# Optimization experiments

Hardware: AMD Instinct MI355X
Metric: run time of the kernel (lower is better)

## Reference

```python
import jax, jax.numpy as jnp
import numpy as np

N, E, F_IN = 10000, 160000, 256
H1, C1 = 8, 128          # conv1: heads=8, out 128 per head, concat -> 1024
H2, C2 = 1, 64           # conv2: heads=1, out 64
NEG_SLOPE = 0.2


def setup_inputs() -> dict:
    key = jax.random.key(0)
    ks = jax.random.split(key, 10)
    s_in = 1.0 / np.sqrt(F_IN)
    s_h1 = 1.0 / np.sqrt(H1 * C1)
    return {
        "x": jax.random.normal(ks[0], (N, F_IN), dtype=jnp.float32),
        "edge_index": jax.random.randint(ks[1], (2, E), 0, N, dtype=jnp.int64),
        "W1": jax.random.normal(ks[2], (F_IN, H1 * C1), dtype=jnp.float32) * s_in,
        "att_src1": jax.random.normal(ks[3], (H1, C1), dtype=jnp.float32) * 0.1,
        "att_dst1": jax.random.normal(ks[4], (H1, C1), dtype=jnp.float32) * 0.1,
        "b1": jnp.zeros((H1 * C1,), dtype=jnp.float32),
        "W2": jax.random.normal(ks[5], (H1 * C1, H2 * C2), dtype=jnp.float32) * s_h1,
        "att_src2": jax.random.normal(ks[6], (H2, C2), dtype=jnp.float32) * 0.1,
        "att_dst2": jax.random.normal(ks[7], (H2, C2), dtype=jnp.float32) * 0.1,
        "b2": jnp.zeros((H2 * C2,), dtype=jnp.float32),
    }


def gat_conv(x, src, dst, W, att_src, att_dst, b, n):
    """PyG GATConv (eval mode: dropout off), concat=True, add_self_loops handled by caller."""
    H, C = att_src.shape
    h = (x @ W).reshape(n, H, C)                       # [N,H,C]
    a_s = jnp.einsum('nhc,hc->nh', h, att_src)         # [N,H]
    a_d = jnp.einsum('nhc,hc->nh', h, att_dst)         # [N,H]
    e = jax.nn.leaky_relu(a_s[src] + a_d[dst], NEG_SLOPE)  # [Etot,H]
    # softmax over edges grouped by destination node (numerically stable)
    e_max = jax.ops.segment_max(e, dst, num_segments=n)
    e = jnp.exp(e - e_max[dst])
    denom = jax.ops.segment_sum(e, dst, num_segments=n)
    alpha = e / (denom[dst] + 1e-16)                   # [Etot,H]
    msg = h[src] * alpha[:, :, None]                   # [Etot,H,C]
    out = jax.ops.segment_sum(msg, dst, num_segments=n)  # [N,H,C]
    return out.reshape(n, H * C) + b


def reference(x, edge_index, W1, att_src1, att_dst1, b1, W2, att_src2, att_dst2, b2):
    n = x.shape[0]
    loops = jnp.arange(n, dtype=edge_index.dtype)
    src = jnp.concatenate([edge_index[0], loops])
    dst = jnp.concatenate([edge_index[1], loops])
    h = jax.nn.elu(gat_conv(x, src, dst, W1, att_src1, att_dst1, b1, n))
    return gat_conv(h, src, dst, W2, att_src2, att_dst2, b2, n)
```

## Files before the change

### kernel.cpp

```cpp
#include <hip/hip_runtime.h>
#include <cmath>


typedef short bf16x8 __attribute__((ext_vector_type(8)));
typedef float f32x4 __attribute__((ext_vector_type(4)));
typedef unsigned short u16x8 __attribute__((ext_vector_type(8)));

__device__ __forceinline__ float lrelu(float x) { return x > 0.f ? x : 0.2f * x; }
__device__ __forceinline__ float b2f(unsigned short h) {
  return __uint_as_float(((unsigned)h) << 16);
}
__device__ __forceinline__ unsigned short f2bf(float f) {
  unsigned u = __float_as_uint(f);
  u += 0x7FFFu + ((u >> 16) & 1u);
  return (unsigned short)(u >> 16);
}

__device__ __forceinline__ void fma8(float* acc, uint4 v, float e) {
  acc[0] += e * __uint_as_float(v.x << 16);
  acc[1] += e * __uint_as_float(v.x & 0xffff0000u);
  acc[2] += e * __uint_as_float(v.y << 16);
  acc[3] += e * __uint_as_float(v.y & 0xffff0000u);
  acc[4] += e * __uint_as_float(v.z << 16);
  acc[5] += e * __uint_as_float(v.z & 0xffff0000u);
  acc[6] += e * __uint_as_float(v.w << 16);
  acc[7] += e * __uint_as_float(v.w & 0xffff0000u);
}

#define GLOAD_LDS16(gsrc, ldst)                                              \
  __builtin_amdgcn_global_load_lds(                                          \
      (const __attribute__((address_space(1))) unsigned int*)(gsrc),         \
      (__attribute__((address_space(3))) unsigned int*)(ldst), 16, 0, 0)


__global__ __launch_bounds__(256) void prep_fused(
    const int* __restrict__ ei, int* __restrict__ counts, int E,
    const float* __restrict__ x, unsigned short* __restrict__ xpk, int N, int MB1,
    const float* __restrict__ W1, unsigned short* __restrict__ w1pk,
    const float* __restrict__ W2, unsigned short* __restrict__ w2pk) {
  const int countB = (E + 255) / 256;
  const int pxB = MB1 * 8;
  int bid = blockIdx.x;
  int t = threadIdx.x;

  if (bid < countB) {
    int e = bid * 256 + t;
    if (e < E) atomicAdd(&counts[ei[E + e]], 1);
    return;
  }
  bid -= countB;
  if (bid < pxB) {
    int mb = bid >> 3, ks = bid & 7;
    int l = t & 63, f = t >> 6;
    int row = mb * 64 + f * 16 + (l & 15);
    int kc = ks * 32 + (l >> 4) * 8;
    float v[8];
#pragma unroll
    for (int j = 0; j < 8; ++j) v[j] = 0.f;
    if (row < N) {
      const float* xr = x + (size_t)row * 256 + kc;
#pragma unroll
      for (int j = 0; j < 8; ++j) v[j] = xr[j];
    }
    u16x8 hi;
#pragma unroll
    for (int j = 0; j < 8; ++j) hi[j] = f2bf(v[j]);
    size_t base = (size_t)(mb * 8 + ks) * 4 * 512;
    *(u16x8*)(xpk + base + (size_t)f * 512 + l * 8) = hi;
    return;
  }
  bid -= pxB;
  if (bid < 64) {
    int hb = bid >> 3, ks = bid & 7;
    int l = t & 63, gq = t >> 6;
    for (int g = gq; g < 8; g += 4) {
      int n = hb * 128 + g * 16 + (l & 15);
      int k0 = ks * 32 + (l >> 4) * 8;
      u16x8 hi, lo;
#pragma unroll
      for (int j = 0; j < 8; ++j) {
        float v = W1[(size_t)(k0 + j) * 1024 + n];
        unsigned short h = f2bf(v);
        hi[j] = h; lo[j] = f2bf(v - b2f(h));
      }
      size_t base = (size_t)(hb * 8 + ks) * 16 * 512;
      *(u16x8*)(w1pk + base + (size_t)g * 512 + l * 8) = hi;
      *(u16x8*)(w1pk + base + (size_t)(8 + g) * 512 + l * 8) = lo;
    }
    return;
  }
  bid -= 64;
  {
    int ks = bid;
    int l = t & 63, g = t >> 6;
    int n = g * 16 + (l & 15);
    int k0 = ks * 32 + (l >> 4) * 8;
    u16x8 hi, lo;
#pragma unroll
    for (int j = 0; j < 8; ++j) {
      float v = W2[(size_t)(k0 + j) * 64 + n];
      unsigned short h = f2bf(v);
      hi[j] = h; lo[j] = f2bf(v - b2f(h));
    }
    size_t base = (size_t)ks * 8 * 512;
    *(u16x8*)(w2pk + base + (size_t)g * 512 + l * 8) = hi;
    *(u16x8*)(w2pk + base + (size_t)(4 + g) * 512 + l * 8) = lo;
  }
}


__global__ __launch_bounds__(256) void scan_blk(const int* __restrict__ counts,
                                                int* __restrict__ offsets,
                                                int* __restrict__ bsum, int n) {
  __shared__ int lds[256];
  int b = blockIdx.x, t = threadIdx.x, i = b * 256 + t;
  int v = (i < n) ? counts[i] + 1 : 0;
  lds[t] = v;
  __syncthreads();
  for (int off = 1; off < 256; off <<= 1) {
    int tv = (t >= off) ? lds[t - off] : 0;
    __syncthreads();
    lds[t] += tv;
    __syncthreads();
  }
  if (i < n) offsets[i] = lds[t] - v;
  if (t == 255) bsum[b] = lds[255];
}

__global__ __launch_bounds__(256) void scan_apply(int* __restrict__ offsets,
                                                  int* __restrict__ cursors,
                                                  const int* __restrict__ bsum,
                                                  int nb, int n) {
  __shared__ int pre_s;
  int b = blockIdx.x, t = threadIdx.x;
  if (t == 0) {
    int s = 0;
    for (int i = 0; i < b; ++i) s += bsum[i];
    pre_s = s;
    if (b == nb - 1) {
      int tot = s;
      for (int i = b; i < nb; ++i) tot += bsum[i];
      offsets[n] = tot;
    }
  }
  __syncthreads();
  int i = b * 256 + t;
  if (i < n) {
    int o = offsets[i] + pre_s;
    offsets[i] = o;
    cursors[i] = o;
  }
}

__global__ __launch_bounds__(256) void fill_all(const int* __restrict__ ei,
                                                int* __restrict__ cursors,
                                                const int* __restrict__ offsets,
                                                int* __restrict__ list,
                                                int E, int n) {
  int tid = blockIdx.x * 256 + threadIdx.x;
  if (tid < E) {
    int d = ei[E + tid];
    int pos = atomicAdd(&cursors[d], 1);
    list[pos] = ei[tid];
  } else if (tid < E + n) {
    int i = tid - E;
    list[offsets[i + 1] - 1] = i;
  }
}


__global__ __launch_bounds__(512, 4) void gemm1_att(
    const unsigned short* __restrict__ xpk, const unsigned short* __restrict__ w1pk,
    const float* __restrict__ asrc, const float* __restrict__ adst,
    unsigned short* __restrict__ h1b, float* __restrict__ as1,
    float* __restrict__ ad1) {
  extern __shared__ char sm[];
  const int t = threadIdx.x, wid = t >> 6, lane = t & 63;
  const int wr = wid >> 2, wc = wid & 3;
  const int mb = blockIdx.x, hb = blockIdx.y;
  const int m0 = mb * 128;
  const int l15 = lane & 15, l4 = lane >> 4;

  f32x4 acc[4][2] = {};

  auto stage = [&](int buf, int ks) {
    char* base0 = sm + buf * 24576;
    for (int i = wid; i < 24; i += 8) {
      const unsigned short* src;
      int ldsoff;
      if (i < 8) {
        int r = i >> 2;
        src = xpk + (size_t)((2 * mb + r) * 8 + ks) * 2048 + (i & 3) * 512 + lane * 8;
        ldsoff = i * 1024;
      } else if (i < 16) {
        int g = i - 8;
        src = w1pk + (size_t)(hb * 8 + ks) * 8192 + g * 512 + lane * 8;
        ldsoff = 8192 + g * 1024;
      } else {
        int g = i - 16;
        src = w1pk + (size_t)(hb * 8 + ks) * 8192 + (8 + g) * 512 + lane * 8;
        ldsoff = 16384 + g * 1024;
      }
      GLOAD_LDS16(src, base0 + ldsoff);
    }
  };

  stage(0, 0);
  __syncthreads();
  int buf = 0;
  for (int step = 0; step < 8; ++step) {
    if (step < 7) stage(buf ^ 1, step + 1);
    const char* b = sm + buf * 24576;
    bf16x8 ah[4], bh[2], bl[2];
#pragma unroll
    for (int mf = 0; mf < 4; ++mf)
      ah[mf] = *(const bf16x8*)(b + (wr * 4 + mf) * 1024 + lane * 16);
#pragma unroll
    for (int nf = 0; nf < 2; ++nf) {
      bh[nf] = *(const bf16x8*)(b + 8192 + (wc * 2 + nf) * 1024 + lane * 16);
      bl[nf] = *(const bf16x8*)(b + 16384 + (wc * 2 + nf) * 1024 + lane * 16);
    }
#pragma unroll
    for (int mf = 0; mf < 4; ++mf)
#pragma unroll
      for (int nf = 0; nf < 2; ++nf) {
        acc[mf][nf] = __builtin_amdgcn_mfma_f32_16x16x32_bf16(ah[mf], bh[nf], acc[mf][nf], 0, 0, 0);
        acc[mf][nf] = __builtin_amdgcn_mfma_f32_16x16x32_bf16(ah[mf], bl[nf], acc[mf][nf], 0, 0, 0);
      }
    __syncthreads();
    buf ^= 1;
  }

  float* parts_s = (float*)sm;
  float* parts_d = (float*)(sm + 2048);
  unsigned short* ctile = (unsigned short*)(sm + 4096);
  float as_c[2], ad_c[2];
#pragma unroll
  for (int nf = 0; nf < 2; ++nf) {
    int col = hb * 128 + wc * 32 + nf * 16 + l15;
    as_c[nf] = asrc[col];
    ad_c[nf] = adst[col];
  }
#pragma unroll
  for (int mf = 0; mf < 4; ++mf) {
    float ss[4] = {0.f, 0.f, 0.f, 0.f}, dd[4] = {0.f, 0.f, 0.f, 0.f};
#pragma unroll
    for (int nf = 0; nf < 2; ++nf)
#pragma unroll
      for (int r = 0; r < 4; ++r) {
        ss[r] += acc[mf][nf][r] * as_c[nf];
        dd[r] += acc[mf][nf][r] * ad_c[nf];
      }
#pragma unroll
    for (int r = 0; r < 4; ++r)
      for (int m = 1; m < 16; m <<= 1) {
        ss[r] += __shfl_xor(ss[r], m);
        dd[r] += __shfl_xor(dd[r], m);
      }
    if (l15 == 0) {
#pragma unroll
      for (int r = 0; r < 4; ++r) {
        int row = wr * 64 + mf * 16 + l4 * 4 + r;
        parts_s[row * 4 + wc] = ss[r];
        parts_d[row * 4 + wc] = dd[r];
      }
    }
#pragma unroll
    for (int nf = 0; nf < 2; ++nf)
#pragma unroll
      for (int r = 0; r < 4; ++r) {
        int row = wr * 64 + mf * 16 + l4 * 4 + r;
        int col = wc * 32 + nf * 16 + l15;
        ctile[row * 128 + col] = f2bf(acc[mf][nf][r]);
      }
  }
  __syncthreads();
  if (t < 128) {
    float s = parts_s[t * 4] + parts_s[t * 4 + 1] + parts_s[t * 4 + 2] + parts_s[t * 4 + 3];
    float d = parts_d[t * 4] + parts_d[t * 4 + 1] + parts_d[t * 4 + 2] + parts_d[t * 4 + 3];
    as1[(size_t)(m0 + t) * 8 + hb] = s;
    ad1[(size_t)(m0 + t) * 8 + hb] = d;
  }
#pragma unroll
  for (int rep = 0; rep < 4; ++rep) {
    int e = rep * 4096 + t * 8;
    int row = e >> 7, col = e & 127;
    bf16x8 v = *(const bf16x8*)(ctile + e);
    *(bf16x8*)(h1b + (size_t)(m0 + row) * 1024 + hb * 128 + col) = v;
  }
}


__global__ __launch_bounds__(256) void agg1_gather(
    const unsigned short* __restrict__ h1b, const float* __restrict__ as1,
    const float* __restrict__ ad1, const int* __restrict__ offsets,
    const int* __restrict__ list, const float* __restrict__ b1,
    unsigned short* __restrict__ o1pk, int n, int nblk) {
  __shared__ __align__(16) unsigned short stg[8192];
  const int t = threadIdx.x, w = t >> 6, lane = t & 63;
  const int h0 = lane >> 4, h1_ = h0 + 4;

  for (int blk = blockIdx.x; blk < nblk; blk += gridDim.x) {
    const int node = blk * 4 + w;
    if (node < n) {
      const int beg = offsets[node], end = offsets[node + 1];
      const float ad0 = ad1[(size_t)node * 8 + h0];
      const float ad4 = ad1[(size_t)node * 8 + h1_];
      float acc0[8] = {}, acc1[8] = {};
      float den0 = 0.f, den4 = 0.f;

      int j = beg;
      int sA = 0, sB = 0;
      float aA0 = 0.f, aA4 = 0.f, aB0 = 0.f, aB4 = 0.f;
      uint4 vA0, vA1, vB0, vB1;
      if (j + 2 <= end) {
        sA = list[j]; sB = list[j + 1];
        aA0 = as1[(size_t)sA * 8 + h0]; aA4 = as1[(size_t)sA * 8 + h1_];
        aB0 = as1[(size_t)sB * 8 + h0]; aB4 = as1[(size_t)sB * 8 + h1_];
        vA0 = *(const uint4*)(h1b + (size_t)sA * 1024 + lane * 8);
        vA1 = *(const uint4*)(h1b + (size_t)sA * 1024 + 512 + lane * 8);
        vB0 = *(const uint4*)(h1b + (size_t)sB * 1024 + lane * 8);
        vB1 = *(const uint4*)(h1b + (size_t)sB * 1024 + 512 + lane * 8);
      }
      for (; j + 4 <= end; j += 2) {
        int sA2 = list[j + 2], sB2 = list[j + 3];
        float aA02 = as1[(size_t)sA2 * 8 + h0], aA42 = as1[(size_t)sA2 * 8 + h1_];
        float aB02 = as1[(size_t)sB2 * 8 + h0], aB42 = as1[(size_t)sB2 * 8 + h1_];
        uint4 nA0 = *(const uint4*)(h1b + (size_t)sA2 * 1024 + lane * 8);
        uint4 nA1 = *(const uint4*)(h1b + (size_t)sA2 * 1024 + 512 + lane * 8);
        uint4 nB0 = *(const uint4*)(h1b + (size_t)sB2 * 1024 + lane * 8);
        uint4 nB1 = *(const uint4*)(h1b + (size_t)sB2 * 1024 + 512 + lane * 8);
        float eA0 = __expf(lrelu(aA0 + ad0)), eA4 = __expf(lrelu(aA4 + ad4));
        float eB0 = __expf(lrelu(aB0 + ad0)), eB4 = __expf(lrelu(aB4 + ad4));
        den0 += eA0 + eB0; den4 += eA4 + eB4;
        fma8(acc0, vA0, eA0); fma8(acc1, vA1, eA4);
        fma8(acc0, vB0, eB0); fma8(acc1, vB1, eB4);
        sA = sA2; sB = sB2;
        aA0 = aA02; aA4 = aA42; aB0 = aB02; aB4 = aB42;
        vA0 = nA0; vA1 = nA1; vB0 = nB0; vB1 = nB1;
      }
      if (j + 2 <= end) {
        float eA0 = __expf(lrelu(aA0 + ad0)), eA4 = __expf(lrelu(aA4 + ad4));
        float eB0 = __expf(lrelu(aB0 + ad0)), eB4 = __expf(lrelu(aB4 + ad4));
        den0 += eA0 + eB0; den4 += eA4 + eB4;
        fma8(acc0, vA0, eA0); fma8(acc1, vA1, eA4);
        fma8(acc0, vB0, eB0); fma8(acc1, vB1, eB4);
        j += 2;
      }
      if (j < end) {
        int s = list[j];
        float a0 = as1[(size_t)s * 8 + h0], a4 = as1[(size_t)s * 8 + h1_];
        uint4 v0 = *(const uint4*)(h1b + (size_t)s * 1024 + lane * 8);
        uint4 v1 = *(const uint4*)(h1b + (size_t)s * 1024 + 512 + lane * 8);
        float e0 = __expf(lrelu(a0 + ad0)), e4 = __expf(lrelu(a4 + ad4));
        den0 += e0; den4 += e4;
        fma8(acc0, v0, e0); fma8(acc1, v1, e4);
      }

      const float inv0 = 1.f / (den0 + 1e-16f);
      const float inv4 = 1.f / (den4 + 1e-16f);
      u16x8 hiA, loA, hiB, loB;
#pragma unroll
      for (int k = 0; k < 8; ++k) {
        float vA = acc0[k] * inv0 + b1[lane * 8 + k];
        float vB = acc1[k] * inv4 + b1[512 + lane * 8 + k];
        vA = vA > 0.f ? vA : expm1f(vA);
        vB = vB > 0.f ? vB : expm1f(vB);
        unsigned short hA = f2bf(vA), hB = f2bf(vB);
        hiA[k] = hA; loA[k] = f2bf(vA - b2f(hA));
        hiB[k] = hB; loB[k] = f2bf(vB - b2f(hB));
      }
      const int q2 = lane >> 2, kc = lane & 3;
      {
        int aw = q2 * 512 + kc * 64 + w * 16;
        *(u16x8*)((char*)stg + (aw ^ ((q2 & 7) << 4))) = hiA;
        aw += 256;
        *(u16x8*)((char*)stg + (aw ^ ((q2 & 7) << 4))) = loA;
      }
      {
        int ks = 16 + q2;
        int aw = ks * 512 + kc * 64 + w * 16;
        *(u16x8*)((char*)stg + (aw ^ ((ks & 7) << 4))) = hiB;
        aw += 256;
        *(u16x8*)((char*)stg + (aw ^ ((ks & 7) << 4))) = loB;
      }
    }
    __syncthreads();
    const int mb = blk >> 4, f = (blk >> 2) & 3, l15b = (blk & 3) * 4;
#pragma unroll
    for (int it = 0; it < 4; ++it) {
      int a = it * 4096 + t * 16;
      int ks = a >> 9, half = (a >> 8) & 1, kcc = (a >> 6) & 3, ww = (a >> 4) & 3;
      u16x8 v = *(const u16x8*)((const char*)stg + (a ^ ((ks & 7) << 4)));
      size_t g = (size_t)(mb * 32 + ks) * 4096 + half * 2048 + (size_t)f * 512 +
                 (size_t)(kcc * 16 + l15b + ww) * 8;
      *(u16x8*)(o1pk + g) = v;
    }
    __syncthreads();
  }
}


__global__ __launch_bounds__(256) void gemm2_splitk(
    const unsigned short* __restrict__ o1pk, const unsigned short* __restrict__ w2pk,
    float* __restrict__ h2p, int Mpad) {
  extern __shared__ char sm[];
  const int t = threadIdx.x, wid = t >> 6, lane = t & 63;
  const int wr = wid >> 1, wc = wid & 1;
  const int mb = blockIdx.x, sk = blockIdx.y;
  const int m0 = mb * 64;
  const int l15 = lane & 15, l4 = lane >> 4;

  f32x4 acc[2][2] = {};

  auto stage = [&](int buf, int ks) {
    char* base0 = sm + buf * 16384;
    const unsigned short* ax = o1pk + (size_t)(mb * 32 + ks) * 8 * 512 + lane * 8;
    for (int i = wid; i < 8; i += 4)
      GLOAD_LDS16(ax + i * 512, base0 + i * 1024);
    const unsigned short* bw = w2pk + (size_t)ks * 8 * 512 + lane * 8;
    for (int i = wid; i < 8; i += 4)
      GLOAD_LDS16(bw + i * 512, base0 + 8192 + i * 1024);
  };

  stage(0, sk * 8);
  __syncthreads();
  int buf = 0;
  for (int step = 0; step < 8; ++step) {
    if (step < 7) stage(buf ^ 1, sk * 8 + step + 1);
    const char* b = sm + buf * 16384;
    bf16x8 ah[2], al[2], bh[2], bl[2];
#pragma unroll
    for (int mf = 0; mf < 2; ++mf) {
      int f = wr * 2 + mf;
      ah[mf] = *(const bf16x8*)(b + f * 1024 + lane * 16);
      al[mf] = *(const bf16x8*)(b + 4096 + f * 1024 + lane * 16);
    }
#pragma unroll
    for (int nf = 0; nf < 2; ++nf) {
      int g = wc * 2 + nf;
      bh[nf] = *(const bf16x8*)(b + 8192 + g * 1024 + lane * 16);
      bl[nf] = *(const bf16x8*)(b + 12288 + g * 1024 + lane * 16);
    }
#pragma unroll
    for (int mf = 0; mf < 2; ++mf)
#pragma unroll
      for (int nf = 0; nf < 2; ++nf) {
        acc[mf][nf] = __builtin_amdgcn_mfma_f32_16x16x32_bf16(ah[mf], bh[nf], acc[mf][nf], 0, 0, 0);
        acc[mf][nf] = __builtin_amdgcn_mfma_f32_16x16x32_bf16(ah[mf], bl[nf], acc[mf][nf], 0, 0, 0);
        acc[mf][nf] = __builtin_amdgcn_mfma_f32_16x16x32_bf16(al[mf], bh[nf], acc[mf][nf], 0, 0, 0);
      }
    __syncthreads();
    buf ^= 1;
  }

#pragma unroll
  for (int mf = 0; mf < 2; ++mf)
#pragma unroll
    for (int nf = 0; nf < 2; ++nf)
#pragma unroll
      for (int r = 0; r < 4; ++r) {
        int row = wr * 32 + mf * 16 + l4 * 4 + r;
        int col = wc * 32 + nf * 16 + l15;
        h2p[((size_t)sk * Mpad + m0 + row) * 64 + col] = acc[mf][nf][r];
      }
}


__global__ __launch_bounds__(256) void reduce_att2(
    const float* __restrict__ h2p, const float* __restrict__ asrc,
    const float* __restrict__ adst, float* __restrict__ h2,
    float* __restrict__ as2, float* __restrict__ ad2, int Mpad, int n) {
  int w = threadIdx.x >> 6, lane = threadIdx.x & 63;
  int row = blockIdx.x * 4 + w;
  if (row >= n) return;
  float s = 0.f;
#pragma unroll
  for (int sk = 0; sk < 4; ++sk) s += h2p[((size_t)sk * Mpad + row) * 64 + lane];
  h2[(size_t)row * 64 + lane] = s;
  float ds = s * asrc[lane], dd = s * adst[lane];
  for (int o = 32; o; o >>= 1) { ds += __shfl_xor(ds, o); dd += __shfl_xor(dd, o); }
  if (lane == 0) { as2[row] = ds; ad2[row] = dd; }
}


__global__ __launch_bounds__(256) void agg2_gather(
    const float* __restrict__ h2, const float* __restrict__ as2,
    const float* __restrict__ ad2, const int* __restrict__ offsets,
    const int* __restrict__ list, const float* __restrict__ b2,
    float* __restrict__ out, int n, int nblk) {
  const int wid = threadIdx.x >> 6, lane = threadIdx.x & 63;
  const int cb = (lane & 15) * 4;
  const int jo = lane >> 4;

  for (int blk = blockIdx.x; blk < nblk; blk += gridDim.x) {
    const int node = blk * 4 + wid;
    if (node >= n) continue;
    const int beg = offsets[node], end = offsets[node + 1];
    const float ad = ad2[node];

    float4 acc = make_float4(0.f, 0.f, 0.f, 0.f);
    float den = 0.f;
    for (int j = beg + jo; j < end; j += 4) {
      int s = list[j];
      float e = __expf(lrelu(as2[s] + ad));
      den += e;
      float4 v = *(const float4*)&h2[(size_t)s * 64 + cb];
      acc.x += e * v.x; acc.y += e * v.y; acc.z += e * v.z; acc.w += e * v.w;
    }
    acc.x += __shfl_xor(acc.x, 16); acc.y += __shfl_xor(acc.y, 16);
    acc.z += __shfl_xor(acc.z, 16); acc.w += __shfl_xor(acc.w, 16);
    den += __shfl_xor(den, 16);
    acc.x += __shfl_xor(acc.x, 32); acc.y += __shfl_xor(acc.y, 32);
    acc.z += __shfl_xor(acc.z, 32); acc.w += __shfl_xor(acc.w, 32);
    den += __shfl_xor(den, 32);
    if (jo == 0) {
      float inv = 1.f / (den + 1e-16f);
      float4 r;
      r.x = acc.x * inv + b2[cb];
      r.y = acc.y * inv + b2[cb + 1];
      r.z = acc.z * inv + b2[cb + 2];
      r.w = acc.w * inv + b2[cb + 3];
      *(float4*)&out[(size_t)node * 64 + cb] = r;
    }
  }
}


extern "C" void kernel_launch(void* const* d_in, const int* in_sizes, int n_in,
                              void* d_out, int out_size, void* d_ws, size_t ws_size,
                              hipStream_t stream) {
  const float* x     = (const float*)d_in[0];
  const int*   ei    = (const int*)d_in[1];
  const float* W1    = (const float*)d_in[2];
  const float* asrc1 = (const float*)d_in[3];
  const float* adst1 = (const float*)d_in[4];
  const float* b1    = (const float*)d_in[5];
  const float* W2    = (const float*)d_in[6];
  const float* asrc2 = (const float*)d_in[7];
  const float* adst2 = (const float*)d_in[8];
  const float* b2    = (const float*)d_in[9];
  float* out = (float*)d_out;

  const int N = in_sizes[0] / 256;
  const int E = in_sizes[1] / 2;
  const int T = E + N;
  const int MBB = (N + 127) / 128;
  const int Mpad = MBB * 128;
  const int MB1 = Mpad / 64;
  const int NB = (N + 255) / 256;
  const int NBLK4 = (N + 3) / 4;
  const int AGG_GRID = NBLK4 < 2048 ? NBLK4 : 2048;

  char* p = (char*)d_ws;
  auto bump = [&](size_t bytes) {
    char* r = p;
    p += (bytes + 255) & ~(size_t)255;
    return r;
  };
  int* counts  = (int*)bump((size_t)N * 4);
  int* offsets = (int*)bump((size_t)(N + 1) * 4);
  int* cursors = (int*)bump((size_t)N * 4);
  int* bsum    = (int*)bump((size_t)NB * 4);
  int* list    = (int*)bump((size_t)T * 4);
  unsigned short* xpk  = (unsigned short*)bump((size_t)Mpad * 256 * 2);
  unsigned short* w1pk = (unsigned short*)bump((size_t)8 * 8 * 16 * 512 * 2);
  unsigned short* h1b  = (unsigned short*)bump((size_t)Mpad * 1024 * 2);
  float* as1           = (float*)bump((size_t)Mpad * 8 * 4);
  float* ad1           = (float*)bump((size_t)Mpad * 8 * 4);
  unsigned short* o1pk = (unsigned short*)bump((size_t)Mpad * 2048 * 2);
  unsigned short* w2pk = (unsigned short*)bump((size_t)32 * 8 * 512 * 2);
  float* as2           = (float*)bump((size_t)Mpad * 4);
  float* ad2           = (float*)bump((size_t)Mpad * 4);
  float* h2p = (float*)h1b;
  float* h2  = (float*)xpk;

  hipMemsetAsync(counts, 0, (size_t)N * 4, stream);
  {
    int gridsz = (E + 255) / 256 + MB1 * 8 + 64 + 32;
    prep_fused<<<gridsz, 256, 0, stream>>>(ei, counts, E, x, xpk, N, MB1,
                                           W1, w1pk, W2, w2pk);
  }
  scan_blk<<<NB, 256, 0, stream>>>(counts, offsets, bsum, N);
  scan_apply<<<NB, 256, 0, stream>>>(offsets, cursors, bsum, NB, N);
  fill_all<<<(E + N + 255) / 256, 256, 0, stream>>>(ei, cursors, offsets, list, E, N);

  gemm1_att<<<dim3(MBB, 8), 512, 49152, stream>>>(xpk, w1pk, asrc1, adst1, h1b, as1, ad1);
  agg1_gather<<<AGG_GRID, 256, 0, stream>>>(h1b, as1, ad1, offsets, list, b1, o1pk, N, NBLK4);

  gemm2_splitk<<<dim3(Mpad / 64, 4), 256, 32768, stream>>>(o1pk, w2pk, h2p, Mpad);
  reduce_att2<<<(N + 3) / 4, 256, 0, stream>>>(h2p, asrc2, adst2, h2, as2, ad2, Mpad, N);
  agg2_gather<<<AGG_GRID, 256, 0, stream>>>(h2, as2, ad2, offsets, list, b2, out, N, NBLK4);
}
```

Before: 156.2 us.

## Replace split-bf16 compensated GEMMs with single-pass fp16 MFMA

```diff
diff --git a/kernel.cpp b/kernel.cpp
--- a/kernel.cpp
+++ b/kernel.cpp
@@ -2,29 +2,28 @@
 #include <cmath>
 
 
-typedef short bf16x8 __attribute__((ext_vector_type(8)));
+typedef _Float16 f16x8 __attribute__((ext_vector_type(8)));
 typedef float f32x4 __attribute__((ext_vector_type(4)));
 typedef unsigned short u16x8 __attribute__((ext_vector_type(8)));
 
 __device__ __forceinline__ float lrelu(float x) { return x > 0.f ? x : 0.2f * x; }
-__device__ __forceinline__ float b2f(unsigned short h) {
-  return __uint_as_float(((unsigned)h) << 16);
-}
-__device__ __forceinline__ unsigned short f2bf(float f) {
-  unsigned u = __float_as_uint(f);
-  u += 0x7FFFu + ((u >> 16) & 1u);
-  return (unsigned short)(u >> 16);
-}
-
-__device__ __forceinline__ void fma8(float* acc, uint4 v, float e) {
-  acc[0] += e * __uint_as_float(v.x << 16);
-  acc[1] += e * __uint_as_float(v.x & 0xffff0000u);
-  acc[2] += e * __uint_as_float(v.y << 16);
-  acc[3] += e * __uint_as_float(v.y & 0xffff0000u);
-  acc[4] += e * __uint_as_float(v.z << 16);
-  acc[5] += e * __uint_as_float(v.z & 0xffff0000u);
-  acc[6] += e * __uint_as_float(v.w << 16);
-  acc[7] += e * __uint_as_float(v.w & 0xffff0000u);
+__device__ __forceinline__ unsigned short f2h(float f) {
+  _Float16 h = (_Float16)f;
+  return __builtin_bit_cast(unsigned short, h);
+}
+__device__ __forceinline__ float h2f(unsigned short u) {
+  return (float)__builtin_bit_cast(_Float16, u);
+}
+
+__device__ __forceinline__ void fma8h(float* acc, uint4 v, float e) {
+  acc[0] += e * h2f((unsigned short)(v.x & 0xffffu));
+  acc[1] += e * h2f((unsigned short)(v.x >> 16));
+  acc[2] += e * h2f((unsigned short)(v.y & 0xffffu));
+  acc[3] += e * h2f((unsigned short)(v.y >> 16));
+  acc[4] += e * h2f((unsigned short)(v.z & 0xffffu));
+  acc[5] += e * h2f((unsigned short)(v.z >> 16));
+  acc[6] += e * h2f((unsigned short)(v.w & 0xffffu));
+  acc[7] += e * h2f((unsigned short)(v.w >> 16));
 }
 
 #define GLOAD_LDS16(gsrc, ldst)                                              \
@@ -62,11 +61,11 @@
 #pragma unroll
       for (int j = 0; j < 8; ++j) v[j] = xr[j];
     }
-    u16x8 hi;
-#pragma unroll
-    for (int j = 0; j < 8; ++j) hi[j] = f2bf(v[j]);
-    size_t base = (size_t)(mb * 8 + ks) * 4 * 512;
-    *(u16x8*)(xpk + base + (size_t)f * 512 + l * 8) = hi;
+    u16x8 hv;
+#pragma unroll
+    for (int j = 0; j < 8; ++j) hv[j] = f2h(v[j]);
+    size_t base = (size_t)(mb * 8 + ks) * 2048;
+    *(u16x8*)(xpk + base + (size_t)f * 512 + l * 8) = hv;
     return;
   }
   bid -= pxB;
@@ -76,16 +75,11 @@
     for (int g = gq; g < 8; g += 4) {
       int n = hb * 128 + g * 16 + (l & 15);
       int k0 = ks * 32 + (l >> 4) * 8;
-      u16x8 hi, lo;
-#pragma unroll
-      for (int j = 0; j < 8; ++j) {
-        float v = W1[(size_t)(k0 + j) * 1024 + n];
-        unsigned short h = f2bf(v);
-        hi[j] = h; lo[j] = f2bf(v - b2f(h));
-      }
-      size_t base = (size_t)(hb * 8 + ks) * 16 * 512;
-      *(u16x8*)(w1pk + base + (size_t)g * 512 + l * 8) = hi;
-      *(u16x8*)(w1pk + base + (size_t)(8 + g) * 512 + l * 8) = lo;
+      u16x8 hv;
+#pragma unroll
+      for (int j = 0; j < 8; ++j) hv[j] = f2h(W1[(size_t)(k0 + j) * 1024 + n]);
+      size_t base = (size_t)(hb * 8 + ks) * 4096;
+      *(u16x8*)(w1pk + base + (size_t)g * 512 + l * 8) = hv;
     }
     return;
   }
@@ -95,16 +89,11 @@
     int l = t & 63, g = t >> 6;
     int n = g * 16 + (l & 15);
     int k0 = ks * 32 + (l >> 4) * 8;
-    u16x8 hi, lo;
-#pragma unroll
-    for (int j = 0; j < 8; ++j) {
-      float v = W2[(size_t)(k0 + j) * 64 + n];
-      unsigned short h = f2bf(v);
-      hi[j] = h; lo[j] = f2bf(v - b2f(h));
-    }
-    size_t base = (size_t)ks * 8 * 512;
-    *(u16x8*)(w2pk + base + (size_t)g * 512 + l * 8) = hi;
-    *(u16x8*)(w2pk + base + (size_t)(4 + g) * 512 + l * 8) = lo;
+    u16x8 hv;
+#pragma unroll
+    for (int j = 0; j < 8; ++j) hv[j] = f2h(W2[(size_t)(k0 + j) * 64 + n]);
+    size_t base = (size_t)ks * 2048;
+    *(u16x8*)(w2pk + base + (size_t)g * 512 + l * 8) = hv;
   }
 }
 
@@ -184,22 +173,18 @@
   f32x4 acc[4][2] = {};
 
   auto stage = [&](int buf, int ks) {
-    char* base0 = sm + buf * 24576;
-    for (int i = wid; i < 24; i += 8) {
+    char* base0 = sm + buf * 16384;
+    for (int i = wid; i < 16; i += 8) {
       const unsigned short* src;
       int ldsoff;
       if (i < 8) {
         int r = i >> 2;
         src = xpk + (size_t)((2 * mb + r) * 8 + ks) * 2048 + (i & 3) * 512 + lane * 8;
         ldsoff = i * 1024;
-      } else if (i < 16) {
+      } else {
         int g = i - 8;
-        src = w1pk + (size_t)(hb * 8 + ks) * 8192 + g * 512 + lane * 8;
+        src = w1pk + (size_t)(hb * 8 + ks) * 4096 + g * 512 + lane * 8;
         ldsoff = 8192 + g * 1024;
-      } else {
-        int g = i - 16;
-        src = w1pk + (size_t)(hb * 8 + ks) * 8192 + (8 + g) * 512 + lane * 8;
-        ldsoff = 16384 + g * 1024;
       }
       GLOAD_LDS16(src, base0 + ldsoff);
     }
@@ -210,23 +195,19 @@
   int buf = 0;
   for (int step = 0; step < 8; ++step) {
     if (step < 7) stage(buf ^ 1, step + 1);
-    const char* b = sm + buf * 24576;
-    bf16x8 ah[4], bh[2], bl[2];
+    const char* b = sm + buf * 16384;
+    f16x8 ah[4], bh[2];
 #pragma unroll
     for (int mf = 0; mf < 4; ++mf)
-      ah[mf] = *(const bf16x8*)(b + (wr * 4 + mf) * 1024 + lane * 16);
-#pragma unroll
-    for (int nf = 0; nf < 2; ++nf) {
-      bh[nf] = *(const bf16x8*)(b + 8192 + (wc * 2 + nf) * 1024 + lane * 16);
-      bl[nf] = *(const bf16x8*)(b + 16384 + (wc * 2 + nf) * 1024 + lane * 16);
-    }
+      ah[mf] = *(const f16x8*)(b + (wr * 4 + mf) * 1024 + lane * 16);
+#pragma unroll
+    for (int nf = 0; nf < 2; ++nf)
+      bh[nf] = *(const f16x8*)(b + 8192 + (wc * 2 + nf) * 1024 + lane * 16);
 #pragma unroll
     for (int mf = 0; mf < 4; ++mf)
 #pragma unroll
-      for (int nf = 0; nf < 2; ++nf) {
-        acc[mf][nf] = __builtin_amdgcn_mfma_f32_16x16x32_bf16(ah[mf], bh[nf], acc[mf][nf], 0, 0, 0);
-        acc[mf][nf] = __builtin_amdgcn_mfma_f32_16x16x32_bf16(ah[mf], bl[nf], acc[mf][nf], 0, 0, 0);
-      }
+      for (int nf = 0; nf < 2; ++nf)
+        acc[mf][nf] = __builtin_amdgcn_mfma_f32_16x16x32_f16(ah[mf], bh[nf], acc[mf][nf], 0, 0, 0);
     __syncthreads();
     buf ^= 1;
   }
@@ -271,7 +252,7 @@
       for (int r = 0; r < 4; ++r) {
         int row = wr * 64 + mf * 16 + l4 * 4 + r;
         int col = wc * 32 + nf * 16 + l15;
-        ctile[row * 128 + col] = f2bf(acc[mf][nf][r]);
+        ctile[row * 128 + col] = f2h(acc[mf][nf][r]);
       }
   }
   __syncthreads();
@@ -285,8 +266,8 @@
   for (int rep = 0; rep < 4; ++rep) {
     int e = rep * 4096 + t * 8;
     int row = e >> 7, col = e & 127;
-    bf16x8 v = *(const bf16x8*)(ctile + e);
-    *(bf16x8*)(h1b + (size_t)(m0 + row) * 1024 + hb * 128 + col) = v;
+    u16x8 v = *(const u16x8*)(ctile + e);
+    *(u16x8*)(h1b + (size_t)(m0 + row) * 1024 + hb * 128 + col) = v;
   }
 }
 
@@ -296,7 +277,7 @@
     const float* __restrict__ ad1, const int* __restrict__ offsets,
     const int* __restrict__ list, const float* __restrict__ b1,
     unsigned short* __restrict__ o1pk, int n, int nblk) {
-  __shared__ __align__(16) unsigned short stg[8192];
+  __shared__ __align__(16) unsigned short stg[4096];
   const int t = threadIdx.x, w = t >> 6, lane = t & 63;
   const int h0 = lane >> 4, h1_ = h0 + 4;
 
@@ -333,8 +314,8 @@
         float eA0 = __expf(lrelu(aA0 + ad0)), eA4 = __expf(lrelu(aA4 + ad4));
         float eB0 = __expf(lrelu(aB0 + ad0)), eB4 = __expf(lrelu(aB4 + ad4));
         den0 += eA0 + eB0; den4 += eA4 + eB4;
-        fma8(acc0, vA0, eA0); fma8(acc1, vA1, eA4);
-        fma8(acc0, vB0, eB0); fma8(acc1, vB1, eB4);
+        fma8h(acc0, vA0, eA0); fma8h(acc1, vA1, eA4);
+        fma8h(acc0, vB0, eB0); fma8h(acc1, vB1, eB4);
         sA = sA2; sB = sB2;
         aA0 = aA02; aA4 = aA42; aB0 = aB02; aB4 = aB42;
         vA0 = nA0; vA1 = nA1; vB0 = nB0; vB1 = nB1;
@@ -343,8 +324,8 @@
         float eA0 = __expf(lrelu(aA0 + ad0)), eA4 = __expf(lrelu(aA4 + ad4));
         float eB0 = __expf(lrelu(aB0 + ad0)), eB4 = __expf(lrelu(aB4 + ad4));
         den0 += eA0 + eB0; den4 += eA4 + eB4;
-        fma8(acc0, vA0, eA0); fma8(acc1, vA1, eA4);
-        fma8(acc0, vB0, eB0); fma8(acc1, vB1, eB4);
+        fma8h(acc0, vA0, eA0); fma8h(acc1, vA1, eA4);
+        fma8h(acc0, vB0, eB0); fma8h(acc1, vB1, eB4);
         j += 2;
       }
       if (j < end) {
@@ -354,45 +335,40 @@
         uint4 v1 = *(const uint4*)(h1b + (size_t)s * 1024 + 512 + lane * 8);
         float e0 = __expf(lrelu(a0 + ad0)), e4 = __expf(lrelu(a4 + ad4));
         den0 += e0; den4 += e4;
-        fma8(acc0, v0, e0); fma8(acc1, v1, e4);
+        fma8h(acc0, v0, e0); fma8h(acc1, v1, e4);
       }
 
       const float inv0 = 1.f / (den0 + 1e-16f);
       const float inv4 = 1.f / (den4 + 1e-16f);
-      u16x8 hiA, loA, hiB, loB;
+      u16x8 hA8, hB8;
 #pragma unroll
       for (int k = 0; k < 8; ++k) {
         float vA = acc0[k] * inv0 + b1[lane * 8 + k];
         float vB = acc1[k] * inv4 + b1[512 + lane * 8 + k];
         vA = vA > 0.f ? vA : expm1f(vA);
         vB = vB > 0.f ? vB : expm1f(vB);
-        unsigned short hA = f2bf(vA), hB = f2bf(vB);
-        hiA[k] = hA; loA[k] = f2bf(vA - b2f(hA));
-        hiB[k] = hB; loB[k] = f2bf(vB - b2f(hB));
+        hA8[k] = f2h(vA);
+        hB8[k] = f2h(vB);
       }
       const int q2 = lane >> 2, kc = lane & 3;
       {
-        int aw = q2 * 512 + kc * 64 + w * 16;
-        *(u16x8*)((char*)stg + (aw ^ ((q2 & 7) << 4))) = hiA;
-        aw += 256;
-        *(u16x8*)((char*)stg + (aw ^ ((q2 & 7) << 4))) = loA;
+        int aw = q2 * 256 + kc * 64 + w * 16;
+        *(u16x8*)((char*)stg + (aw ^ ((q2 & 7) << 4))) = hA8;
       }
       {
         int ks = 16 + q2;
-        int aw = ks * 512 + kc * 64 + w * 16;
-        *(u16x8*)((char*)stg + (aw ^ ((ks & 7) << 4))) = hiB;
-        aw += 256;
-        *(u16x8*)((char*)stg + (aw ^ ((ks & 7) << 4))) = loB;
+        int aw = ks * 256 + kc * 64 + w * 16;
+        *(u16x8*)((char*)stg + (aw ^ ((ks & 7) << 4))) = hB8;
       }
     }
     __syncthreads();
     const int mb = blk >> 4, f = (blk >> 2) & 3, l15b = (blk & 3) * 4;
 #pragma unroll
-    for (int it = 0; it < 4; ++it) {
+    for (int it = 0; it < 2; ++it) {
       int a = it * 4096 + t * 16;
-      int ks = a >> 9, half = (a >> 8) & 1, kcc = (a >> 6) & 3, ww = (a >> 4) & 3;
+      int ks = a >> 8, kcc = (a >> 6) & 3, ww = (a >> 4) & 3;
       u16x8 v = *(const u16x8*)((const char*)stg + (a ^ ((ks & 7) << 4)));
-      size_t g = (size_t)(mb * 32 + ks) * 4096 + half * 2048 + (size_t)f * 512 +
+      size_t g = (size_t)(mb * 32 + ks) * 2048 + (size_t)f * 512 +
                  (size_t)(kcc * 16 + l15b + ww) * 8;
       *(u16x8*)(o1pk + g) = v;
     }
@@ -414,13 +390,16 @@
   f32x4 acc[2][2] = {};
 
   auto stage = [&](int buf, int ks) {
-    char* base0 = sm + buf * 16384;
-    const unsigned short* ax = o1pk + (size_t)(mb * 32 + ks) * 8 * 512 + lane * 8;
-    for (int i = wid; i < 8; i += 4)
+    char* base0 = sm + buf * 8192;
+    const unsigned short* ax = o1pk + (size_t)(mb * 32 + ks) * 2048 + lane * 8;
+    for (int i = wid; i < 4; i += 4)
       GLOAD_LDS16(ax + i * 512, base0 + i * 1024);
-    const unsigned short* bw = w2pk + (size_t)ks * 8 * 512 + lane * 8;
-    for (int i = wid; i < 8; i += 4)
-      GLOAD_LDS16(bw + i * 512, base0 + 8192 + i * 1024);
+    if (wid >= 0) {
+      int i = wid;
+      GLOAD_LDS16(ax + i * 512, base0 + i * 1024);
+      const unsigned short* bw = w2pk + (size_t)ks * 2048 + lane * 8;
+      GLOAD_LDS16(bw + i * 512, base0 + 4096 + i * 1024);
+    }
   };
 
   stage(0, sk * 8);
@@ -428,28 +407,19 @@
   int buf = 0;
   for (int step = 0; step < 8; ++step) {
     if (step < 7) stage(buf ^ 1, sk * 8 + step + 1);
-    const char* b = sm + buf * 16384;
-    bf16x8 ah[2], al[2], bh[2], bl[2];
-#pragma unroll
-    for (int mf = 0; mf < 2; ++mf) {
-      int f = wr * 2 + mf;
-      ah[mf] = *(const bf16x8*)(b + f * 1024 + lane * 16);
-      al[mf] = *(const bf16x8*)(b + 4096 + f * 1024 + lane * 16);
-    }
-#pragma unroll
-    for (int nf = 0; nf < 2; ++nf) {
-      int g = wc * 2 + nf;
-      bh[nf] = *(const bf16x8*)(b + 8192 + g * 1024 + lane * 16);
-      bl[nf] = *(const bf16x8*)(b + 12288 + g * 1024 + lane * 16);
-    }
+    const char* b = sm + buf * 8192;
+    f16x8 ah[2], bh[2];
 #pragma unroll
     for (int mf = 0; mf < 2; ++mf)
-#pragma unroll
-      for (int nf = 0; nf < 2; ++nf) {
-        acc[mf][nf] = __builtin_amdgcn_mfma_f32_16x16x32_bf16(ah[mf], bh[nf], acc[mf][nf], 0, 0, 0);
-        acc[mf][nf] = __builtin_amdgcn_mfma_f32_16x16x32_bf16(ah[mf], bl[nf], acc[mf][nf], 0, 0, 0);
-        acc[mf][nf] = __builtin_amdgcn_mfma_f32_16x16x32_bf16(al[mf], bh[nf], acc[mf][nf], 0, 0, 0);
-      }
+      ah[mf] = *(const f16x8*)(b + (wr * 2 + mf) * 1024 + lane * 16);
+#pragma unroll
+    for (int nf = 0; nf < 2; ++nf)
+      bh[nf] = *(const f16x8*)(b + 4096 + (wc * 2 + nf) * 1024 + lane * 16);
+#pragma unroll
+    for (int mf = 0; mf < 2; ++mf)
+#pragma unroll
+      for (int nf = 0; nf < 2; ++nf)
+        acc[mf][nf] = __builtin_amdgcn_mfma_f32_16x16x32_f16(ah[mf], bh[nf], acc[mf][nf], 0, 0, 0);
     __syncthreads();
     buf ^= 1;
   }
@@ -564,12 +534,12 @@
   int* bsum    = (int*)bump((size_t)NB * 4);
   int* list    = (int*)bump((size_t)T * 4);
   unsigned short* xpk  = (unsigned short*)bump((size_t)Mpad * 256 * 2);
-  unsigned short* w1pk = (unsigned short*)bump((size_t)8 * 8 * 16 * 512 * 2);
+  unsigned short* w1pk = (unsigned short*)bump((size_t)1024 * 256 * 2);
   unsigned short* h1b  = (unsigned short*)bump((size_t)Mpad * 1024 * 2);
   float* as1           = (float*)bump((size_t)Mpad * 8 * 4);
   float* ad1           = (float*)bump((size_t)Mpad * 8 * 4);
-  unsigned short* o1pk = (unsigned short*)bump((size_t)Mpad * 2048 * 2);
-  unsigned short* w2pk = (unsigned short*)bump((size_t)32 * 8 * 512 * 2);
+  unsigned short* o1pk = (unsigned short*)bump((size_t)Mpad * 1024 * 2);
+  unsigned short* w2pk = (unsigned short*)bump((size_t)64 * 1024 * 2);
   float* as2           = (float*)bump((size_t)Mpad * 4);
   float* ad2           = (float*)bump((size_t)Mpad * 4);
   float* h2p = (float*)h1b;
@@ -585,10 +555,10 @@
   scan_apply<<<NB, 256, 0, stream>>>(offsets, cursors, bsum, NB, N);
   fill_all<<<(E + N + 255) / 256, 256, 0, stream>>>(ei, cursors, offsets, list, E, N);
 
-  gemm1_att<<<dim3(MBB, 8), 512, 49152, stream>>>(xpk, w1pk, asrc1, adst1, h1b, as1, ad1);
+  gemm1_att<<<dim3(MBB, 8), 512, 36864, stream>>>(xpk, w1pk, asrc1, adst1, h1b, as1, ad1);
   agg1_gather<<<AGG_GRID, 256, 0, stream>>>(h1b, as1, ad1, offsets, list, b1, o1pk, N, NBLK4);
 
-  gemm2_splitk<<<dim3(Mpad / 64, 4), 256, 32768, stream>>>(o1pk, w2pk, h2p, Mpad);
+  gemm2_splitk<<<dim3(Mpad / 64, 4), 256, 16384, stream>>>(o1pk, w2pk, h2p, Mpad);
   reduce_att2<<<(N + 3) / 4, 256, 0, stream>>>(h2p, asrc2, adst2, h2, as2, ad2, Mpad, N);
   agg2_gather<<<AGG_GRID, 256, 0, stream>>>(h2, as2, ad2, offsets, list, b2, out, N, NBLK4);
 }
```

Result: faster. 145.4 us (-6.9%).
